# Optimization experiments

Measured on AMD Instinct MI355X. Metric: run time of the kernel, lower is better.

The kernel has to match this reference:

```python
import jax, jax.numpy as jnp
import numpy as np

B, N, LAT, H, NL, NH = 1, 512, 128, 256, 3, 4
EMB = H // 4  # atom-type embedding dim = 64
DH = H // NH  # head dim = 64
LN_EPS = 1e-5


def _lin(x, w, b):
    # torch nn.Linear convention: w is (out, in)
    return x @ w.T + b


def _ln(x, s, b):
    m = jnp.mean(x, -1, keepdims=True)
    v = jnp.mean((x - m) ** 2, -1, keepdims=True)
    return (x - m) / jnp.sqrt(v + LN_EPS) * s + b


def setup_inputs() -> dict:
    key = jax.random.key(0)
    ks = iter(jax.random.split(key, 64))
    def w(shape, scale=0.02):
        return (jax.random.normal(next(ks), shape, jnp.float32) * scale).astype(jnp.float32)
    inp = dict(
        z=jax.random.normal(next(ks), (B, N, LAT), jnp.float32),
        z_global=jax.random.normal(next(ks), (B, LAT), jnp.float32),
        atom_types=jax.random.randint(next(ks), (B, N), 0, 4),
        emb=w((4, EMB), 1.0),
        ip_w1=w((H, LAT + EMB)), ip_b1=jnp.zeros(H), ip_w2=w((H, H)), ip_b2=jnp.zeros(H),
        gp_w1=w((H, LAT)), gp_b1=jnp.zeros(H), gp_w2=w((H, H)), gp_b2=jnp.zeros(H),
        tf_wqkv=w((NL, 3 * H, H)), tf_bqkv=jnp.zeros((NL, 3 * H)),
        tf_wo=w((NL, H, H)), tf_bo=jnp.zeros((NL, H)),
        tf_ln1_s=jnp.ones((NL, H)), tf_ln1_b=jnp.zeros((NL, H)),
        tf_w1=w((NL, 4 * H, H)), tf_b1=jnp.zeros((NL, 4 * H)),
        tf_w2=w((NL, H, 4 * H)), tf_b2=jnp.zeros((NL, H)),
        tf_ln2_s=jnp.ones((NL, H)), tf_ln2_b=jnp.zeros((NL, H)),
        dp_w1=w((H, 2 * H)), dp_b1=jnp.zeros(H), dp_w2=w((H, H)), dp_b2=jnp.zeros(H),
        dp_w3=w((1, H)), dp_b3=jnp.zeros(1),
        cp_w1=w((H, H)), cp_b1=jnp.zeros(H), cp_w2=w((3, H)), cp_b2=jnp.zeros(3),
    )
    return inp


def _forward(z, z_global, atom_types, emb,
             ip_w1, ip_b1, ip_w2, ip_b2,
             gp_w1, gp_b1, gp_w2, gp_b2,
             tf_wqkv, tf_bqkv, tf_wo, tf_bo, tf_ln1_s, tf_ln1_b,
             tf_w1, tf_b1, tf_w2, tf_b2, tf_ln2_s, tf_ln2_b,
             dp_w1, dp_b1, dp_w2, dp_b2, dp_w3, dp_b3,
             cp_w1, cp_b1, cp_w2, cp_b2):
    Bs, Ns = z.shape[0], z.shape[1]
    atom_feats = emb[atom_types]                      # (B,N,EMB)
    z_input = jnp.concatenate([z, atom_feats], -1)    # (B,N,LAT+EMB)
    h = _lin(jax.nn.silu(_lin(z_input, ip_w1, ip_b1)), ip_w2, ip_b2)
    g = _lin(jax.nn.silu(_lin(z_global, gp_w1, gp_b1)), gp_w2, gp_b2)
    h = h + g[:, None, :]
    # post-norm TransformerEncoder (relu FFN, eval mode -> no dropout)
    scale = 1.0 / np.sqrt(DH)
    for l in range(NL):
        qkv = _lin(h, tf_wqkv[l], tf_bqkv[l])
        q, k, v = jnp.split(qkv, 3, -1)
        q = q.reshape(Bs, Ns, NH, DH)
        k = k.reshape(Bs, Ns, NH, DH)
        v = v.reshape(Bs, Ns, NH, DH)
        att = jax.nn.softmax(jnp.einsum('bqhd,bkhd->bhqk', q, k) * scale, -1)
        o = jnp.einsum('bhqk,bkhd->bqhd', att, v).reshape(Bs, Ns, H)
        h = _ln(h + _lin(o, tf_wo[l], tf_bo[l]), tf_ln1_s[l], tf_ln1_b[l])
        ff = _lin(jax.nn.relu(_lin(h, tf_w1[l], tf_b1[l])), tf_w2[l], tf_b2[l])
        h = _ln(h + ff, tf_ln2_s[l], tf_ln2_b[l])
    # dist head: Linear(concat(h_i,h_j)) == h_i @ W[:, :H].T + h_j @ W[:, H:].T + b
    # (avoids materializing the (B,N,N,2H) concat; identical math)
    ai = h @ dp_w1[:, :H].T                           # (B,N,H)
    aj = h @ dp_w1[:, H:].T                           # (B,N,H)
    pair = jax.nn.silu(ai[:, :, None, :] + aj[:, None, :, :] + dp_b1)  # (B,N,N,H)
    pair = jax.nn.silu(_lin(pair, dp_w2, dp_b2))
    dist = jax.nn.softplus(_lin(pair, dp_w3, dp_b3))[..., 0]           # (B,N,N)
    dist = (dist + jnp.swapaxes(dist, 1, 2)) * 0.5
    x = _lin(jax.nn.silu(_lin(h, cp_w1, cp_b1)), cp_w2, cp_b2)          # (B,N,3)
    return x, dist


def reference(z, z_global, atom_types, emb,
              ip_w1, ip_b1, ip_w2, ip_b2,
              gp_w1, gp_b1, gp_w2, gp_b2,
              tf_wqkv, tf_bqkv, tf_wo, tf_bo, tf_ln1_s, tf_ln1_b,
              tf_w1, tf_b1, tf_w2, tf_b2, tf_ln2_s, tf_ln2_b,
              dp_w1, dp_b1, dp_w2, dp_b2, dp_w3, dp_b3,
              cp_w1, cp_b1, cp_w2, cp_b2):
    return _forward(z, z_global, atom_types, emb,
                    ip_w1, ip_b1, ip_w2, ip_b2,
                    gp_w1, gp_b1, gp_w2, gp_b2,
                    tf_wqkv, tf_bqkv, tf_wo, tf_bo, tf_ln1_s, tf_ln1_b,
                    tf_w1, tf_b1, tf_w2, tf_b2, tf_ln2_s, tf_ln2_b,
                    dp_w1, dp_b1, dp_w2, dp_b2, dp_w3, dp_b3,
                    cp_w1, cp_b1, cp_w2, cp_b2)
```

## Files before the change

kernel.cpp:

```cpp
#include <hip/hip_runtime.h>
#include <hip/hip_bf16.h>
#include <cstdint>

typedef __bf16 bf16;
typedef __attribute__((ext_vector_type(8))) __bf16 bf16x8;
typedef __attribute__((ext_vector_type(4))) float f32x4;

__device__ __forceinline__ float fast_rcp(float x) { return __builtin_amdgcn_rcpf(x); }
__device__ __forceinline__ float silu_f(float x) { return x * fast_rcp(1.f + __expf(-x)); }
__device__ __forceinline__ bf16x8 cvt8(float4 a, float4 b) {
  bf16x8 o;
  o[0]=(bf16)a.x; o[1]=(bf16)a.y; o[2]=(bf16)a.z; o[3]=(bf16)a.w;
  o[4]=(bf16)b.x; o[5]=(bf16)b.y; o[6]=(bf16)b.z; o[7]=(bf16)b.w;
  return o;
}

constexpr long WB_IPW1 = 0;
constexpr long WB_IPW2 = 49152;
constexpr long WB_QKV  = 114688;
constexpr long WB_WO   = 704512;
constexpr long WB_W1   = 901120;
constexpr long WB_W2   = 1687552;
constexpr long WB_DPW1 = 2473984;
constexpr long WB_DPW2 = 2605056;
constexpr long WB_CPW1 = 2670592;
constexpr long F_ZIN = 5472256;
constexpr long F_G   = F_ZIN + 512L*192*4;
constexpr long F_H   = F_G + 1024;
constexpr long F_QKV = F_H + 512L*256*4;
constexpr long F_S   = F_QKV + 512L*768*4;
constexpr long F_VT  = F_S + 4L*512*512*4;
constexpr long F_O   = F_VT + 4L*64*512*2;
constexpr long F_T1  = F_O + 512L*256*4;
constexpr long O_W2P  = F_T1 + 512L*256*4;
constexpr long O_WDP  = O_W2P + 131072;
constexpr long O_B512 = O_WDP + 262144;

__global__ __launch_bounds__(256) void prep_kernel(
    const float* __restrict__ s_ipw1, const float* __restrict__ s_ipw2,
    const float* __restrict__ s_qkv,  const float* __restrict__ s_wo,
    const float* __restrict__ s_w1,   const float* __restrict__ s_w2,
    const float* __restrict__ s_dpw1, const float* __restrict__ s_dpw2,
    const float* __restrict__ s_cpw1, bf16* __restrict__ dst,
    const float* __restrict__ z, const int* __restrict__ at, const float* __restrict__ emb,
    const float* __restrict__ zg, const float* __restrict__ gw1, const float* __restrict__ gb1,
    const float* __restrict__ gw2, const float* __restrict__ gb2,
    const float* __restrict__ dpb1,
    float* __restrict__ zi, bf16* __restrict__ w2p, bf16* __restrict__ wdp,
    float* __restrict__ g, float* __restrict__ bias512)
{
  __shared__ float zs[128];
  __shared__ float ts[256];
  const int b = blockIdx.x, tid = threadIdx.x;
  if (b < 2672) {
    long v = (long)b * 256 + tid;
    if (v >= 684032) return;
    const float* src; long off;
    if (v < 176128) {
      if (v < 12288)      { src = s_ipw1; off = 0; }
      else if (v < 28672) { src = s_ipw2; off = 12288; }
      else                { src = s_qkv;  off = 28672; }
    } else if (v < 618496) {
      if (v < 225280)      { src = s_wo; off = 176128; }
      else if (v < 421888) { src = s_w1; off = 225280; }
      else                 { src = s_w2; off = 421888; }
    } else {
      if (v < 651264)      { src = s_dpw1; off = 618496; }
      else if (v < 667648) { src = s_dpw2; off = 651264; }
      else                 { src = s_cpw1; off = 667648; }
    }
    long e = (v - off) * 4;
    float4 f = *(const float4*)&src[e];
    bf16* d = dst + off * 4 + e;
    d[0] = (bf16)f.x; d[1] = (bf16)f.y; d[2] = (bf16)f.z; d[3] = (bf16)f.w;
  } else if (b < 3056) {
    int idx = (b - 2672) * 256 + tid;
    int n = idx / 192, c = idx - n * 192;
    zi[idx] = (c < 128) ? z[n * 128 + c] : emb[at[n] * 64 + (c - 128)];
  } else if (b < 3088) {
    int f = (b - 3056) * 256 + tid;
    int l15 = f & 15, kq = (f >> 4) & 3, ks = (f >> 6) & 7, nt = f >> 9;
    int n = nt * 16 + l15, k0 = ks * 32 + kq * 8;
    float4 v0 = *(const float4*)&s_dpw2[n * 256 + k0];
    float4 v1 = *(const float4*)&s_dpw2[n * 256 + k0 + 4];
    *(bf16x8*)&w2p[(long)f * 8] = cvt8(v0, v1);
  } else if (b < 3216) {
    int v = (b - 3088) * 256 + tid;
    int r = v >> 6, c4 = (v & 63) << 2;
    long src = (r < 256) ? ((long)r * 512 + c4) : ((long)(r - 256) * 512 + 256 + c4);
    float4 f = *(const float4*)&s_dpw1[src];
    bf16* d = &wdp[r * 256 + c4];
    d[0]=(bf16)f.x; d[1]=(bf16)f.y; d[2]=(bf16)f.z; d[3]=(bf16)f.w;
  } else if (b == 3216) {
    if (tid < 128) zs[tid] = zg[tid];
    __syncthreads();
    float s = gb1[tid];
    for (int k = 0; k < 128; ++k) s += zs[k] * gw1[tid * 128 + k];
    ts[tid] = silu_f(s);
    __syncthreads();
    float s2 = gb2[tid];
    for (int k = 0; k < 256; ++k) s2 += ts[k] * gw2[tid * 256 + k];
    g[tid] = s2;
  } else {
    bias512[tid] = dpb1[tid];
    bias512[256 + tid] = 0.f;
  }
}

template<int ACT, typename WT>
__global__ __launch_bounds__(256) void gemm_kernel(
    const float* __restrict__ A, int lda, long sA,
    const WT* __restrict__ W, int ldw, long sW,
    const float* __restrict__ bias,
    const float* __restrict__ R, int ldr, long sR,
    float* __restrict__ C, int ldc, long sC, int K)
{
  const int bz = blockIdx.z;
  A += (long)bz * sA;  W += (long)bz * sW;  C += (long)bz * sC;
  if (R) R += (long)bz * sR;
  const int m0 = blockIdx.x * 64, n0 = blockIdx.y * 64;
  __shared__ bf16 As[64][72];
  __shared__ bf16 Ws[64][72];
  const int tid = threadIdx.x;
  const int lane = tid & 63, wid = tid >> 6;
  const int wm = (wid & 1) * 32, wn = (wid >> 1) * 32;
  const int rr = lane & 15, kg = (lane >> 4) << 3;
  f32x4 acc[2][2] = {};
  for (int k0 = 0; k0 < K; k0 += 64) {
#pragma unroll
    for (int r = 0; r < 4; ++r) {
      int lin = tid + r * 256;
      int row = lin >> 4, kc = (lin & 15) << 2;
      {
        const float* p = &A[(long)(m0 + row) * lda + k0 + kc];
        float4 v = *(const float4*)p;
        As[row][kc] = (bf16)v.x; As[row][kc + 1] = (bf16)v.y;
        As[row][kc + 2] = (bf16)v.z; As[row][kc + 3] = (bf16)v.w;
      }
      {
        const WT* p = &W[(long)(n0 + row) * ldw + k0 + kc];
        if constexpr (sizeof(WT) == 4) {
          float4 v = *(const float4*)p;
          Ws[row][kc] = (bf16)v.x; Ws[row][kc + 1] = (bf16)v.y;
          Ws[row][kc + 2] = (bf16)v.z; Ws[row][kc + 3] = (bf16)v.w;
        } else {
          *(uint2*)&Ws[row][kc] = *(const uint2*)p;
        }
      }
    }
    __syncthreads();
#pragma unroll
    for (int ks = 0; ks < 2; ++ks) {
      const int kk = ks * 32 + kg;
      bf16x8 a0 = *(const bf16x8*)&As[wm + rr][kk];
      bf16x8 a1 = *(const bf16x8*)&As[wm + 16 + rr][kk];
      bf16x8 b0 = *(const bf16x8*)&Ws[wn + rr][kk];
      bf16x8 b1 = *(const bf16x8*)&Ws[wn + 16 + rr][kk];
      acc[0][0] = __builtin_amdgcn_mfma_f32_16x16x32_bf16(a0, b0, acc[0][0], 0, 0, 0);
      acc[0][1] = __builtin_amdgcn_mfma_f32_16x16x32_bf16(a0, b1, acc[0][1], 0, 0, 0);
      acc[1][0] = __builtin_amdgcn_mfma_f32_16x16x32_bf16(a1, b0, acc[1][0], 0, 0, 0);
      acc[1][1] = __builtin_amdgcn_mfma_f32_16x16x32_bf16(a1, b1, acc[1][1], 0, 0, 0);
    }
    __syncthreads();
  }
  const int rg = lane >> 4;
#pragma unroll
  for (int mi = 0; mi < 2; ++mi)
#pragma unroll
    for (int ni = 0; ni < 2; ++ni)
#pragma unroll
      for (int r = 0; r < 4; ++r) {
        int gm = m0 + wm + mi * 16 + rg * 4 + r;
        int gn = n0 + wn + ni * 16 + rr;
        float v = acc[mi][ni][r];
        if (bias) v += bias[gn];
        if (R) v += R[(long)gm * ldr + gn];
        if (ACT == 1) v = silu_f(v);
        else if (ACT == 2) v = fmaxf(v, 0.f);
        C[(long)gm * ldc + gn] = v;
      }
}

__global__ __launch_bounds__(256) void softmax_kernel(float* __restrict__ S)
{
  long base = ((long)blockIdx.y * 512 + blockIdx.x) * 512;
  float* row = S + base;
  int tid = threadIdx.x;
  float a = row[tid] * 0.125f, b = row[tid + 256] * 0.125f;
  float m = fmaxf(a, b);
#pragma unroll
  for (int o = 1; o < 64; o <<= 1) m = fmaxf(m, __shfl_xor(m, o));
  __shared__ float red[4];
  __shared__ float red2[4];
  int wid = tid >> 6;
  if ((tid & 63) == 0) red[wid] = m;
  __syncthreads();
  m = fmaxf(fmaxf(red[0], red[1]), fmaxf(red[2], red[3]));
  float e0 = __expf(a - m), e1 = __expf(b - m);
  float s = e0 + e1;
#pragma unroll
  for (int o = 1; o < 64; o <<= 1) s += __shfl_xor(s, o);
  if ((tid & 63) == 0) red2[wid] = s;
  __syncthreads();
  s = red2[0] + red2[1] + red2[2] + red2[3];
  float inv = fast_rcp(s);
  row[tid] = e0 * inv; row[tid + 256] = e1 * inv;
}

__global__ __launch_bounds__(256) void vt_kernel(const float* __restrict__ qkv, bf16* __restrict__ vt)
{
  int idx = blockIdx.x * 256 + threadIdx.x;
  int hh = idx >> 15;
  int r = idx & 32767;
  int d = r >> 9, n = r & 511;
  vt[idx] = (bf16)qkv[(long)n * 768 + 512 + hh * 64 + d];
}

__global__ __launch_bounds__(256) void ln_kernel(
    const float* __restrict__ X, const float* __restrict__ sc,
    const float* __restrict__ bi, float* __restrict__ Y)
{
  int row = blockIdx.x, tid = threadIdx.x;
  float v = X[(long)row * 256 + tid];
  float s = v;
#pragma unroll
  for (int o = 1; o < 64; o <<= 1) s += __shfl_xor(s, o);
  __shared__ float r1[4];
  __shared__ float r2[4];
  if ((tid & 63) == 0) r1[tid >> 6] = s;
  __syncthreads();
  float mean = (r1[0] + r1[1] + r1[2] + r1[3]) * (1.f / 256.f);
  float d = v - mean;
  float t = d * d;
#pragma unroll
  for (int o = 1; o < 64; o <<= 1) t += __shfl_xor(t, o);
  if ((tid & 63) == 0) r2[tid >> 6] = t;
  __syncthreads();
  float var = (r2[0] + r2[1] + r2[2] + r2[3]) * (1.f / 256.f);
  Y[(long)row * 256 + tid] = d * rsqrtf(var + 1e-5f) * sc[tid] + bi[tid];
}

__global__ __launch_bounds__(256, 2) void pair2_kernel(
    const float* __restrict__ ai, const float* __restrict__ aj,
    const bf16* __restrict__ W2P, const float* __restrict__ b2g,
    const float* __restrict__ w3g, const float* __restrict__ b3p,
    float* __restrict__ dout)
{
  __shared__ float ai_s[256];
  __shared__ bf16  t_s[64 * 256];
  __shared__ float part[64][4];
  const int tid = threadIdx.x, lane = tid & 63, w = tid >> 6;
  const int l15 = lane & 15, kq = lane >> 4;
  const int i = blockIdx.x >> 1, half = blockIdx.x & 1;
  const float b3v = b3p[0];

  ai_s[tid] = ai[(long)i * 512 + tid];

  bf16x8 w2r[4][8];
  float b2v[4], w3v[4];
#pragma unroll
  for (int nt = 0; nt < 4; ++nt) {
    int ntg = w * 4 + nt;
#pragma unroll
    for (int ks = 0; ks < 8; ++ks)
      w2r[nt][ks] = *(const bf16x8*)&W2P[(long)((((ntg * 8 + ks) * 4 + kq) * 16) + l15) * 8];
    b2v[nt] = b2g[ntg * 16 + l15];
    w3v[nt] = w3g[ntg * 16 + l15];
  }
  __syncthreads();

  for (int jc = half * 4; jc < half * 4 + 4; ++jc) {
    const int j0 = jc * 64;
    const float* ajp = aj + (long)(j0 + lane) * 512;
#pragma unroll
    for (int r = 0; r < 8; ++r) {
      int kk = w + 4 * r;
      float4 a0 = *(const float4*)(ajp + kk * 8);
      float4 a1 = *(const float4*)(ajp + kk * 8 + 4);
      const float* aip = ai_s + kk * 8;
      bf16x8 tv;
      tv[0] = (bf16)silu_f(a0.x + aip[0]); tv[1] = (bf16)silu_f(a0.y + aip[1]);
      tv[2] = (bf16)silu_f(a0.z + aip[2]); tv[3] = (bf16)silu_f(a0.w + aip[3]);
      tv[4] = (bf16)silu_f(a1.x + aip[4]); tv[5] = (bf16)silu_f(a1.y + aip[5]);
      tv[6] = (bf16)silu_f(a1.z + aip[6]); tv[7] = (bf16)silu_f(a1.w + aip[7]);
      *(bf16x8*)&t_s[(kk * 64 + lane) * 8] = tv;
    }
    __syncthreads();

    f32x4 acc[4][4] = {};
#pragma unroll
    for (int ks = 0; ks < 8; ++ks) {
      bf16x8 af[4];
#pragma unroll
      for (int Mt = 0; Mt < 4; ++Mt)
        af[Mt] = *(const bf16x8*)&t_s[((ks * 4 + kq) * 64 + Mt * 16 + l15) * 8];
#pragma unroll
      for (int nt = 0; nt < 4; ++nt)
#pragma unroll
        for (int Mt = 0; Mt < 4; ++Mt)
          acc[Mt][nt] = __builtin_amdgcn_mfma_f32_16x16x32_bf16(af[Mt], w2r[nt][ks], acc[Mt][nt], 0, 0, 0);
    }

#pragma unroll
    for (int Mt = 0; Mt < 4; ++Mt)
#pragma unroll
      for (int r = 0; r < 4; ++r) {
        float s = silu_f(acc[Mt][0][r] + b2v[0]) * w3v[0]
                + silu_f(acc[Mt][1][r] + b2v[1]) * w3v[1]
                + silu_f(acc[Mt][2][r] + b2v[2]) * w3v[2]
                + silu_f(acc[Mt][3][r] + b2v[3]) * w3v[3];
        s += __shfl_xor(s, 1); s += __shfl_xor(s, 2);
        s += __shfl_xor(s, 4); s += __shfl_xor(s, 8);
        if (l15 == 0) part[Mt * 16 + kq * 4 + r][w] = s;
      }
    __syncthreads();
    if (tid < 64) {
      float s = part[tid][0] + part[tid][1] + part[tid][2] + part[tid][3] + b3v;
      float dd = fmaxf(s, 0.f) + log1pf(__expf(-fabsf(s)));
      dout[(long)i * 512 + j0 + tid] = dd;
    }
    __syncthreads();
  }
}

__global__ __launch_bounds__(256) void sym_kernel(float* __restrict__ dist)
{
  int idx = blockIdx.x * 256 + threadIdx.x;
  int i = idx >> 9, j = idx & 511;
  if (i < j) {
    float a = dist[idx];
    float b = dist[(long)j * 512 + i];
    float m = 0.5f * (a + b);
    dist[idx] = m;
    dist[(long)j * 512 + i] = m;
  }
}

__global__ __launch_bounds__(256) void coord_kernel(
    const float* __restrict__ ct, const float* __restrict__ w2,
    const float* __restrict__ b2, float* __restrict__ out)
{
  int t = blockIdx.x * 256 + threadIdx.x;
  if (t >= 1536) return;
  int row = t / 3, c = t - row * 3;
  float s = b2[c];
  const float* a = &ct[(long)row * 256];
  const float* wp = &w2[c * 256];
  for (int k = 0; k < 256; ++k) s += a[k] * wp[k];
  out[t] = s;
}

extern "C" void kernel_launch(void* const* d_in, const int* in_sizes, int n_in,
                              void* d_out, int out_size, void* d_ws, size_t ws_size,
                              hipStream_t stream) {
  const float* z        = (const float*)d_in[0];
  const float* z_global = (const float*)d_in[1];
  const int*   atom_t   = (const int*)d_in[2];
  const float* emb      = (const float*)d_in[3];
  const float* ip_w1 = (const float*)d_in[4];  const float* ip_b1 = (const float*)d_in[5];
  const float* ip_w2 = (const float*)d_in[6];  const float* ip_b2 = (const float*)d_in[7];
  const float* gp_w1 = (const float*)d_in[8];  const float* gp_b1 = (const float*)d_in[9];
  const float* gp_w2 = (const float*)d_in[10]; const float* gp_b2 = (const float*)d_in[11];
  const float* wqkv  = (const float*)d_in[12]; const float* bqkv  = (const float*)d_in[13];
  const float* wo    = (const float*)d_in[14]; const float* bo    = (const float*)d_in[15];
  const float* ln1s  = (const float*)d_in[16]; const float* ln1b  = (const float*)d_in[17];
  const float* w1    = (const float*)d_in[18]; const float* b1    = (const float*)d_in[19];
  const float* w2    = (const float*)d_in[20]; const float* b2    = (const float*)d_in[21];
  const float* ln2s  = (const float*)d_in[22]; const float* ln2b  = (const float*)d_in[23];
  const float* dpw1  = (const float*)d_in[24]; const float* dpb1  = (const float*)d_in[25];
  const float* dpw2  = (const float*)d_in[26]; const float* dpb2  = (const float*)d_in[27];
  const float* dpw3  = (const float*)d_in[28]; const float* dpb3  = (const float*)d_in[29];
  const float* cpw1  = (const float*)d_in[30]; const float* cpb1  = (const float*)d_in[31];
  const float* cpw2  = (const float*)d_in[32]; const float* cpb2  = (const float*)d_in[33];

  char* ws = (char*)d_ws;
  bf16*  WB   = (bf16*)ws;
  float* zin  = (float*)(ws + F_ZIN);
  float* g    = (float*)(ws + F_G);
  float* h    = (float*)(ws + F_H);
  float* qkv  = (float*)(ws + F_QKV);
  float* S    = (float*)(ws + F_S);
  bf16*  Vt   = (bf16*)(ws + F_VT);
  float* o    = (float*)(ws + F_O);
  float* t1   = (float*)(ws + F_T1);
  bf16*  W2P  = (bf16*)(ws + O_W2P);
  bf16*  WDP  = (bf16*)(ws + O_WDP);
  float* b512 = (float*)(ws + O_B512);
  float* ff1  = S;
  float* aiaj = S;
  float* out  = (float*)d_out;
  float* xout = out;
  float* dist = out + 1536;

  prep_kernel<<<3218, 256, 0, stream>>>(ip_w1, ip_w2, wqkv, wo, w1, w2, dpw1, dpw2, cpw1, WB,
      z, atom_t, emb, z_global, gp_w1, gp_b1, gp_w2, gp_b2, dpb1,
      zin, W2P, WDP, g, b512);

  gemm_kernel<1, bf16><<<dim3(8, 4, 1), 256, 0, stream>>>(zin, 192, 0, WB + WB_IPW1, 192, 0,
      ip_b1, nullptr, 0, 0, t1, 256, 0, 192);
  gemm_kernel<0, bf16><<<dim3(8, 4, 1), 256, 0, stream>>>(t1, 256, 0, WB + WB_IPW2, 256, 0,
      ip_b2, g, 0, 0, h, 256, 0, 256);

  for (int l = 0; l < 3; ++l) {
    const bf16* wq = WB + WB_QKV + (long)l * 768 * 256;
    gemm_kernel<0, bf16><<<dim3(8, 12, 1), 256, 0, stream>>>(h, 256, 0, wq, 256, 0,
        bqkv + l * 768, nullptr, 0, 0, qkv, 768, 0, 256);
    gemm_kernel<0, float><<<dim3(8, 8, 4), 256, 0, stream>>>(qkv, 768, 64, qkv + 256, 768, 64,
        nullptr, nullptr, 0, 0, S, 512, 262144, 64);
    softmax_kernel<<<dim3(512, 4), 256, 0, stream>>>(S);
    vt_kernel<<<512, 256, 0, stream>>>(qkv, Vt);
    gemm_kernel<0, bf16><<<dim3(8, 1, 4), 256, 0, stream>>>(S, 512, 262144, Vt, 512, 32768,
        nullptr, nullptr, 0, 0, o, 256, 64, 512);
    gemm_kernel<0, bf16><<<dim3(8, 4, 1), 256, 0, stream>>>(o, 256, 0,
        WB + WB_WO + (long)l * 65536, 256, 0, bo + l * 256, h, 256, 0, t1, 256, 0, 256);
    ln_kernel<<<512, 256, 0, stream>>>(t1, ln1s + l * 256, ln1b + l * 256, h);
    gemm_kernel<2, bf16><<<dim3(8, 16, 1), 256, 0, stream>>>(h, 256, 0,
        WB + WB_W1 + (long)l * 262144, 256, 0, b1 + l * 1024, nullptr, 0, 0, ff1, 1024, 0, 256);
    gemm_kernel<0, bf16><<<dim3(8, 4, 1), 256, 0, stream>>>(ff1, 1024, 0,
        WB + WB_W2 + (long)l * 262144, 1024, 0, b2 + l * 256, h, 256, 0, t1, 256, 0, 1024);
    ln_kernel<<<512, 256, 0, stream>>>(t1, ln2s + l * 256, ln2b + l * 256, h);
  }

  gemm_kernel<0, bf16><<<dim3(8, 8, 1), 256, 0, stream>>>(h, 256, 0, WDP, 256, 0,
      b512, nullptr, 0, 0, aiaj, 512, 0, 256);
  pair2_kernel<<<1024, 256, 0, stream>>>(aiaj, aiaj + 256, W2P, dpb2, dpw3, dpb3, dist);
  sym_kernel<<<1024, 256, 0, stream>>>(dist);
  gemm_kernel<1, bf16><<<dim3(8, 4, 1), 256, 0, stream>>>(h, 256, 0, WB + WB_CPW1, 256, 0,
      cpb1, nullptr, 0, 0, t1, 256, 0, 256);
  coord_kernel<<<6, 256, 0, stream>>>(t1, cpw2, cpb2, xout);
}
```

Before: 375.2 us.

## Fuse V-transpose into QKV GEMM, softmax into PV, split pair work finer

The QKV projection now writes Q/K into a compact buffer and scatters V directly as a transposed bf16 tensor, which removes the separate vt_kernel. Softmax is fused with the P·V product: each block normalizes one attention row in shared memory and does a scalar dot-product with Vt, so the normalized scores are never written back and there is no separate PV GEMM launch. The pair kernel grid doubles so each block handles two j-chunks instead of four, which adds parallelism but makes each block reload the W2 fragments. The V scatter writes are uncoalesced, and the PV stage swaps MFMA for scalar FMAs.

Result: slower. 393.3 us (+4.8%).

```diff
diff --git a/kernel.cpp b/kernel.cpp
--- a/kernel.cpp
+++ b/kernel.cpp
@@ -5,6 +5,8 @@
 typedef __bf16 bf16;
 typedef __attribute__((ext_vector_type(8))) __bf16 bf16x8;
 typedef __attribute__((ext_vector_type(4))) float f32x4;
+
+#define MFMA16(a, b, c) __builtin_amdgcn_mfma_f32_16x16x32_bf16(a, b, c, 0, 0, 0)
 
 __device__ __forceinline__ float fast_rcp(float x) { return __builtin_amdgcn_rcpf(x); }
 __device__ __forceinline__ float silu_f(float x) { return x * fast_rcp(1.f + __expf(-x)); }
@@ -21,8 +23,6 @@
 constexpr long WB_WO   = 704512;
 constexpr long WB_W1   = 901120;
 constexpr long WB_W2   = 1687552;
-constexpr long WB_DPW1 = 2473984;
-constexpr long WB_DPW2 = 2605056;
 constexpr long WB_CPW1 = 2670592;
 constexpr long F_ZIN = 5472256;
 constexpr long F_G   = F_ZIN + 512L*192*4;
@@ -156,10 +156,10 @@
       bf16x8 a1 = *(const bf16x8*)&As[wm + 16 + rr][kk];
       bf16x8 b0 = *(const bf16x8*)&Ws[wn + rr][kk];
       bf16x8 b1 = *(const bf16x8*)&Ws[wn + 16 + rr][kk];
-      acc[0][0] = __builtin_amdgcn_mfma_f32_16x16x32_bf16(a0, b0, acc[0][0], 0, 0, 0);
-      acc[0][1] = __builtin_amdgcn_mfma_f32_16x16x32_bf16(a0, b1, acc[0][1], 0, 0, 0);
-      acc[1][0] = __builtin_amdgcn_mfma_f32_16x16x32_bf16(a1, b0, acc[1][0], 0, 0, 0);
-      acc[1][1] = __builtin_amdgcn_mfma_f32_16x16x32_bf16(a1, b1, acc[1][1], 0, 0, 0);
+      acc[0][0] = MFMA16(a0, b0, acc[0][0]);
+      acc[0][1] = MFMA16(a0, b1, acc[0][1]);
+      acc[1][0] = MFMA16(a1, b0, acc[1][0]);
+      acc[1][1] = MFMA16(a1, b1, acc[1][1]);
     }
     __syncthreads();
   }
@@ -181,17 +181,81 @@
       }
 }
 
-__global__ __launch_bounds__(256) void softmax_kernel(float* __restrict__ S)
-{
-  long base = ((long)blockIdx.y * 512 + blockIdx.x) * 512;
-  float* row = S + base;
-  int tid = threadIdx.x;
-  float a = row[tid] * 0.125f, b = row[tid + 256] * 0.125f;
-  float m = fmaxf(a, b);
-#pragma unroll
-  for (int o = 1; o < 64; o <<= 1) m = fmaxf(m, __shfl_xor(m, o));
+__global__ __launch_bounds__(256) void gemm_qkv_kernel(
+    const float* __restrict__ A,
+    const bf16* __restrict__ W,
+    const float* __restrict__ bias,
+    float* __restrict__ qk, bf16* __restrict__ vt)
+{
+  const int m0 = blockIdx.x * 64, n0 = blockIdx.y * 64;
+  __shared__ bf16 As[64][72];
+  __shared__ bf16 Ws[64][72];
+  const int tid = threadIdx.x;
+  const int lane = tid & 63, wid = tid >> 6;
+  const int wm = (wid & 1) * 32, wn = (wid >> 1) * 32;
+  const int rr = lane & 15, kg = (lane >> 4) << 3;
+  f32x4 acc[2][2] = {};
+  for (int k0 = 0; k0 < 256; k0 += 64) {
+#pragma unroll
+    for (int r = 0; r < 4; ++r) {
+      int lin = tid + r * 256;
+      int row = lin >> 4, kc = (lin & 15) << 2;
+      {
+        const float* p = &A[(long)(m0 + row) * 256 + k0 + kc];
+        float4 v = *(const float4*)p;
+        As[row][kc] = (bf16)v.x; As[row][kc + 1] = (bf16)v.y;
+        As[row][kc + 2] = (bf16)v.z; As[row][kc + 3] = (bf16)v.w;
+      }
+      *(uint2*)&Ws[row][kc] = *(const uint2*)&W[(long)(n0 + row) * 256 + k0 + kc];
+    }
+    __syncthreads();
+#pragma unroll
+    for (int ks = 0; ks < 2; ++ks) {
+      const int kk = ks * 32 + kg;
+      bf16x8 a0 = *(const bf16x8*)&As[wm + rr][kk];
+      bf16x8 a1 = *(const bf16x8*)&As[wm + 16 + rr][kk];
+      bf16x8 b0 = *(const bf16x8*)&Ws[wn + rr][kk];
+      bf16x8 b1 = *(const bf16x8*)&Ws[wn + 16 + rr][kk];
+      acc[0][0] = MFMA16(a0, b0, acc[0][0]);
+      acc[0][1] = MFMA16(a0, b1, acc[0][1]);
+      acc[1][0] = MFMA16(a1, b0, acc[1][0]);
+      acc[1][1] = MFMA16(a1, b1, acc[1][1]);
+    }
+    __syncthreads();
+  }
+  const int rg = lane >> 4;
+#pragma unroll
+  for (int mi = 0; mi < 2; ++mi)
+#pragma unroll
+    for (int ni = 0; ni < 2; ++ni)
+#pragma unroll
+      for (int r = 0; r < 4; ++r) {
+        int gm = m0 + wm + mi * 16 + rg * 4 + r;
+        int gn = n0 + wn + ni * 16 + rr;
+        float v = acc[mi][ni][r] + bias[gn];
+        if (gn < 512) {
+          qk[(long)gm * 512 + gn] = v;
+        } else {
+          int c = gn - 512;
+          vt[(long)(c >> 6) * 32768 + (long)(c & 63) * 512 + gm] = (bf16)v;
+        }
+      }
+}
+
+__global__ __launch_bounds__(256) void softmax_pv_kernel(
+    const float* __restrict__ S, const bf16* __restrict__ Vt, float* __restrict__ o)
+{
+  const int row = blockIdx.x, h = blockIdx.y;
+  const float* srow = S + ((long)h * 512 + row) * 512;
+  __shared__ float p_s[512];
   __shared__ float red[4];
   __shared__ float red2[4];
+  __shared__ float part[64][4];
+  const int tid = threadIdx.x;
+  float a = srow[tid] * 0.125f, b = srow[tid + 256] * 0.125f;
+  float m = fmaxf(a, b);
+#pragma unroll
+  for (int t = 1; t < 64; t <<= 1) m = fmaxf(m, __shfl_xor(m, t));
   int wid = tid >> 6;
   if ((tid & 63) == 0) red[wid] = m;
   __syncthreads();
@@ -199,21 +263,29 @@
   float e0 = __expf(a - m), e1 = __expf(b - m);
   float s = e0 + e1;
 #pragma unroll
-  for (int o = 1; o < 64; o <<= 1) s += __shfl_xor(s, o);
+  for (int t = 1; t < 64; t <<= 1) s += __shfl_xor(s, t);
   if ((tid & 63) == 0) red2[wid] = s;
   __syncthreads();
   s = red2[0] + red2[1] + red2[2] + red2[3];
   float inv = fast_rcp(s);
-  row[tid] = e0 * inv; row[tid + 256] = e1 * inv;
-}
-
-__global__ __launch_bounds__(256) void vt_kernel(const float* __restrict__ qkv, bf16* __restrict__ vt)
-{
-  int idx = blockIdx.x * 256 + threadIdx.x;
-  int hh = idx >> 15;
-  int r = idx & 32767;
-  int d = r >> 9, n = r & 511;
-  vt[idx] = (bf16)qkv[(long)n * 768 + 512 + hh * 64 + d];
+  p_s[tid] = e0 * inv; p_s[tid + 256] = e1 * inv;
+  __syncthreads();
+  const int d = tid & 63, kc = tid >> 6;
+  const bf16* vp = Vt + (long)h * 32768 + (long)d * 512 + kc * 128;
+  const float* pp = &p_s[kc * 128];
+  float acc = 0.f;
+#pragma unroll
+  for (int k = 0; k < 128; k += 8) {
+    bf16x8 vv = *(const bf16x8*)&vp[k];
+    acc += pp[k]     * (float)vv[0] + pp[k + 1] * (float)vv[1]
+         + pp[k + 2] * (float)vv[2] + pp[k + 3] * (float)vv[3]
+         + pp[k + 4] * (float)vv[4] + pp[k + 5] * (float)vv[5]
+         + pp[k + 6] * (float)vv[6] + pp[k + 7] * (float)vv[7];
+  }
+  part[d][kc] = acc;
+  __syncthreads();
+  if (tid < 64)
+    o[(long)row * 256 + h * 64 + tid] = part[tid][0] + part[tid][1] + part[tid][2] + part[tid][3];
 }
 
 __global__ __launch_bounds__(256) void ln_kernel(
@@ -251,7 +323,7 @@
   __shared__ float part[64][4];
   const int tid = threadIdx.x, lane = tid & 63, w = tid >> 6;
   const int l15 = lane & 15, kq = lane >> 4;
-  const int i = blockIdx.x >> 1, half = blockIdx.x & 1;
+  const int i = blockIdx.x >> 2, q = blockIdx.x & 3;
   const float b3v = b3p[0];
 
   ai_s[tid] = ai[(long)i * 512 + tid];
@@ -269,7 +341,7 @@
   }
   __syncthreads();
 
-  for (int jc = half * 4; jc < half * 4 + 4; ++jc) {
+  for (int jc = q * 2; jc < q * 2 + 2; ++jc) {
     const int j0 = jc * 64;
     const float* ajp = aj + (long)(j0 + lane) * 512;
 #pragma unroll
@@ -298,7 +370,7 @@
       for (int nt = 0; nt < 4; ++nt)
 #pragma unroll
         for (int Mt = 0; Mt < 4; ++Mt)
-          acc[Mt][nt] = __builtin_amdgcn_mfma_f32_16x16x32_bf16(af[Mt], w2r[nt][ks], acc[Mt][nt], 0, 0, 0);
+          acc[Mt][nt] = MFMA16(af[Mt], w2r[nt][ks], acc[Mt][nt]);
     }
 
 #pragma unroll
@@ -378,7 +450,7 @@
   float* zin  = (float*)(ws + F_ZIN);
   float* g    = (float*)(ws + F_G);
   float* h    = (float*)(ws + F_H);
-  float* qkv  = (float*)(ws + F_QKV);
+  float* qk   = (float*)(ws + F_QKV);
   float* S    = (float*)(ws + F_S);
   bf16*  Vt   = (bf16*)(ws + F_VT);
   float* o    = (float*)(ws + F_O);
@@ -402,15 +474,11 @@
       ip_b2, g, 0, 0, h, 256, 0, 256);
 
   for (int l = 0; l < 3; ++l) {
-    const bf16* wq = WB + WB_QKV + (long)l * 768 * 256;
-    gemm_kernel<0, bf16><<<dim3(8, 12, 1), 256, 0, stream>>>(h, 256, 0, wq, 256, 0,
-        bqkv + l * 768, nullptr, 0, 0, qkv, 768, 0, 256);
-    gemm_kernel<0, float><<<dim3(8, 8, 4), 256, 0, stream>>>(qkv, 768, 64, qkv + 256, 768, 64,
+    gemm_qkv_kernel<<<dim3(8, 12), 256, 0, stream>>>(h,
+        WB + WB_QKV + (long)l * 196608, bqkv + l * 768, qk, Vt);
+    gemm_kernel<0, float><<<dim3(8, 8, 4), 256, 0, stream>>>(qk, 512, 64, qk + 256, 512, 64,
         nullptr, nullptr, 0, 0, S, 512, 262144, 64);
-    softmax_kernel<<<dim3(512, 4), 256, 0, stream>>>(S);
-    vt_kernel<<<512, 256, 0, stream>>>(qkv, Vt);
-    gemm_kernel<0, bf16><<<dim3(8, 1, 4), 256, 0, stream>>>(S, 512, 262144, Vt, 512, 32768,
-        nullptr, nullptr, 0, 0, o, 256, 64, 512);
+    softmax_pv_kernel<<<dim3(512, 4), 256, 0, stream>>>(S, Vt, o);
     gemm_kernel<0, bf16><<<dim3(8, 4, 1), 256, 0, stream>>>(o, 256, 0,
         WB + WB_WO + (long)l * 65536, 256, 0, bo + l * 256, h, 256, 0, t1, 256, 0, 256);
     ln_kernel<<<512, 256, 0, stream>>>(t1, ln1s + l * 256, ln1b + l * 256, h);
@@ -423,7 +491,7 @@
 
   gemm_kernel<0, bf16><<<dim3(8, 8, 1), 256, 0, stream>>>(h, 256, 0, WDP, 256, 0,
       b512, nullptr, 0, 0, aiaj, 512, 0, 256);
-  pair2_kernel<<<1024, 256, 0, stream>>>(aiaj, aiaj + 256, W2P, dpb2, dpw3, dpb3, dist);
+  pair2_kernel<<<2048, 256, 0, stream>>>(aiaj, aiaj + 256, W2P, dpb2, dpw3, dpb3, dist);
   sym_kernel<<<1024, 256, 0, stream>>>(dist);
   gemm_kernel<1, bf16><<<dim3(8, 4, 1), 256, 0, stream>>>(h, 256, 0, WB + WB_CPW1, 256, 0,
       cpb1, nullptr, 0, 0, t1, 256, 0, 256);
```
